# Kernel tuning notes

Hardware: AMD Instinct MI355X
Metric: run time of the kernel (lower is better)

Reference implementation:

```python
import jax, jax.numpy as jnp
import numpy as np

B, T, C = 2, 2048, 1024
H = 16
HD = C // H  # head_size = 64
FF = 2 * C   # ffwd_size default = n_embd * 2
EPS = float(jnp.finfo(jnp.float32).eps)  # torch RMSNorm eps=None -> finfo eps


def rmsnorm(x, g):
    # torch.nn.RMSNorm: x / sqrt(mean(x^2) + eps) * weight
    ms = jnp.mean(jnp.square(x), axis=-1, keepdims=True)
    return x * jax.lax.rsqrt(ms + EPS) * g


def setup_inputs() -> dict:
    key = jax.random.key(0)
    ks = jax.random.split(key, 12)
    s_in = 1.0 / np.sqrt(C)
    s_ff = 1.0 / np.sqrt(FF)
    return {
        "target": jax.random.normal(ks[0], (B, T, C), dtype=jnp.float32),
        # per-head projections, torch Linear layout [out, in] stacked over heads: [H, HD, C]
        "wq": jax.random.uniform(ks[1], (H, HD, C), jnp.float32, -s_in, s_in),
        "wk": jax.random.uniform(ks[2], (H, HD, C), jnp.float32, -s_in, s_in),
        "wv": jax.random.uniform(ks[3], (H, HD, C), jnp.float32, -s_in, s_in),
        "w_proj": jax.random.uniform(ks[4], (C, H * HD), jnp.float32, -s_in, s_in),
        "b_proj": jax.random.uniform(ks[5], (C,), jnp.float32, -s_in, s_in),
        "w1": jax.random.uniform(ks[6], (FF, C), jnp.float32, -s_in, s_in),
        "b1": jax.random.uniform(ks[7], (FF,), jnp.float32, -s_in, s_in),
        "w2": jax.random.uniform(ks[8], (C, FF), jnp.float32, -s_ff, s_ff),
        "b2": jax.random.uniform(ks[9], (C,), jnp.float32, -s_ff, s_ff),
        "g1": jnp.ones((C,), jnp.float32),
        "g2": jnp.ones((C,), jnp.float32),
    }


def reference(target, wq, wk, wv, w_proj, b_proj, w1, b1, w2, b2, g1, g2):
    x = rmsnorm(target, g1)
    # q,k,v: [B,H,T,HD]
    q = jnp.einsum("btc,hdc->bhtd", x, wq)
    k = jnp.einsum("btc,hdc->bhtd", x, wk)
    v = jnp.einsum("btc,hdc->bhtd", x, wv)
    scale = HD ** -0.5
    wei = jnp.einsum("bhtd,bhsd->bhts", q, k) * scale  # [B,H,T,T]
    causal = jnp.tril(jnp.ones((T, T), dtype=bool))
    wei = jnp.where(causal, wei, -jnp.inf)
    wei = jax.nn.softmax(wei, axis=-1)
    attn = jnp.einsum("bhts,bhsd->bhtd", wei, v)  # [B,H,T,HD]
    attn = attn.transpose(0, 2, 1, 3).reshape(B, T, H * HD)  # concat heads
    attn = attn @ w_proj.T + b_proj
    target = target + attn
    y = rmsnorm(target, g2)
    h = jax.nn.gelu(y @ w1.T + b1, approximate=False)  # torch nn.GELU default = exact
    ff = h @ w2.T + b2
    return target + ff
```

## Files before the change

kernel.cpp:

```cpp
#include <hip/hip_runtime.h>
#include <math.h>

#define B_  2
#define T_  2048
#define C_  1024
#define H_  16
#define HD_ 64
#define FF_ 2048
#define EPS_ 1.1920929e-07f

typedef __attribute__((ext_vector_type(8))) short short8;
typedef __attribute__((ext_vector_type(4))) float f32x4;

__device__ __forceinline__ unsigned short f2bf(float f) {
    unsigned u = __float_as_uint(f);
    u += 0x7fffu + ((u >> 16) & 1u);
    return (unsigned short)(u >> 16);
}
__device__ __forceinline__ float bf2f(unsigned short u) {
    return __uint_as_float(((unsigned)u) << 16);
}

__global__ void prep_kernel(const float* __restrict__ wq, const float* __restrict__ wk,
                            const float* __restrict__ wv, const float* __restrict__ wp,
                            const float* __restrict__ w1, const float* __restrict__ w2,
                            unsigned short* __restrict__ wb,
                            const float* __restrict__ x, const float* __restrict__ g,
                            unsigned short* __restrict__ y) {
    int tid = threadIdx.x;
    if (blockIdx.x < 8192) {
        size_t i = ((size_t)blockIdx.x * 256 + tid) * 4;
        const float* src; size_t off = i;
        if      (i < 1048576u)  { src = wq; }
        else if (i < 2097152u)  { src = wk; off = i - 1048576u; }
        else if (i < 3145728u)  { src = wv; off = i - 2097152u; }
        else if (i < 4194304u)  { src = wp; off = i - 3145728u; }
        else if (i < 6291456u)  { src = w1; off = i - 4194304u; }
        else                    { src = w2; off = i - 6291456u; }
        float4 v4 = *(const float4*)(src + off);
        ushort4 o4;
        o4.x = f2bf(v4.x); o4.y = f2bf(v4.y); o4.z = f2bf(v4.z); o4.w = f2bf(v4.w);
        *(ushort4*)(wb + i) = o4;
    } else {
        int row = blockIdx.x - 8192;
        const float4* xr = (const float4*)(x + (size_t)row * C_);
        float4 xv = xr[tid];
        float ss = xv.x * xv.x + xv.y * xv.y + xv.z * xv.z + xv.w * xv.w;
        #pragma unroll
        for (int m = 32; m >= 1; m >>= 1) ss += __shfl_xor(ss, m, 64);
        __shared__ float sred[4];
        if ((tid & 63) == 0) sred[tid >> 6] = ss;
        __syncthreads();
        float tot = sred[0] + sred[1] + sred[2] + sred[3];
        float r = rsqrtf(tot * (1.0f / C_) + EPS_);
        float4 gv = ((const float4*)g)[tid];
        ushort4 o;
        o.x = f2bf(xv.x * r * gv.x);
        o.y = f2bf(xv.y * r * gv.y);
        o.z = f2bf(xv.z * r * gv.z);
        o.w = f2bf(xv.w * r * gv.w);
        *((ushort4*)(y + (size_t)row * C_) + tid) = o;
    }
}

__global__ void rmsnorm_bf16_kernel(const float* __restrict__ x, const float* __restrict__ g,
                                    unsigned short* __restrict__ y) {
    int row = blockIdx.x;
    int tid = threadIdx.x;
    const float4* xr = (const float4*)(x + (size_t)row * C_);
    float4 xv = xr[tid];
    float ss = xv.x * xv.x + xv.y * xv.y + xv.z * xv.z + xv.w * xv.w;
    #pragma unroll
    for (int m = 32; m >= 1; m >>= 1) ss += __shfl_xor(ss, m, 64);
    __shared__ float sred[4];
    if ((tid & 63) == 0) sred[tid >> 6] = ss;
    __syncthreads();
    float tot = sred[0] + sred[1] + sred[2] + sred[3];
    float r = rsqrtf(tot * (1.0f / C_) + EPS_);
    float4 gv = ((const float4*)g)[tid];
    ushort4 o;
    o.x = f2bf(xv.x * r * gv.x);
    o.y = f2bf(xv.y * r * gv.y);
    o.z = f2bf(xv.z * r * gv.z);
    o.w = f2bf(xv.w * r * gv.w);
    *((ushort4*)(y + (size_t)row * C_) + tid) = o;
}

template <int TM, int ACT, bool BIAS, bool RES, bool OBF16, int ROUTE>
__global__ __launch_bounds__(256) void mfma_gemm(
        const unsigned short* __restrict__ A, const unsigned short* __restrict__ W,
        const float* __restrict__ bias, const float* __restrict__ resid,
        void* __restrict__ O0, void* __restrict__ O1, void* __restrict__ O2,
        int M, int N, int K) {
    constexpr int ACH = TM / 8;
    constexpr int NCH = (ACH + 16) / 4;
    constexpr int MI  = TM / 32;
    __shared__ short As[2 * TM * 32];
    __shared__ short Bs[2 * 128 * 32];
    const int tid  = threadIdx.x;
    const int w    = tid >> 6, lane = tid & 63;
    const int tileN = blockIdx.x * 128, tileM = blockIdx.y * TM;

    const unsigned short* gsrc[NCH];
    short* ldst[NCH];
    #pragma unroll
    for (int i2 = 0; i2 < NCH; ++i2) {
        int c = w * NCH + i2;
        if (c < ACH) {
            int kh = c / (ACH / 2), lc = c % (ACH / 2);
            gsrc[i2] = A + (size_t)(tileM + lc * 16 + (lane >> 2)) * K + kh * 32 + (lane & 3) * 8;
            ldst[i2] = As + c * 512;
        } else {
            int c2 = c - ACH;
            int kh = c2 >> 3, lc = c2 & 7;
            gsrc[i2] = W + (size_t)(tileN + lc * 16 + (lane >> 2)) * K + kh * 32 + (lane & 3) * 8;
            ldst[i2] = Bs + c2 * 512;
        }
    }

    f32x4 acc[MI][4];
    const f32x4 zed = {0.f, 0.f, 0.f, 0.f};
    #pragma unroll
    for (int i = 0; i < MI; ++i)
        #pragma unroll
        for (int j = 0; j < 4; ++j) acc[i][j] = zed;

    const int wm = (w >> 1) * (TM / 2), wn = (w & 1) * 64;
    const int frow = lane & 15, koff = (lane >> 4) * 8;

    for (int k0 = 0; k0 < K; k0 += 64) {
        #pragma unroll
        for (int i2 = 0; i2 < NCH; ++i2)
            __builtin_amdgcn_global_load_lds(
                (const __attribute__((address_space(1))) unsigned*)(gsrc[i2] + k0),
                (__attribute__((address_space(3))) unsigned*)ldst[i2], 16, 0, 0);
        __syncthreads();

        #pragma unroll
        for (int kh = 0; kh < 2; ++kh) {
            short8 af[MI], bfr[4];
            #pragma unroll
            for (int i = 0; i < MI; ++i)
                af[i] = *(const short8*)(As + kh * TM * 32 + (wm + i * 16 + frow) * 32 + koff);
            #pragma unroll
            for (int j = 0; j < 4; ++j)
                bfr[j] = *(const short8*)(Bs + kh * 128 * 32 + (wn + j * 16 + frow) * 32 + koff);
            #pragma unroll
            for (int i = 0; i < MI; ++i)
                #pragma unroll
                for (int j = 0; j < 4; ++j)
                    acc[i][j] = __builtin_amdgcn_mfma_f32_16x16x32_bf16(af[i], bfr[j], acc[i][j], 0, 0, 0);
        }
        __syncthreads();
    }

    const int ecol = lane & 15, erow = (lane >> 4) * 4;
    const int zone = ROUTE ? (tileN >> 10) : 0;
    #pragma unroll
    for (int j = 0; j < 4; ++j) {
        int n = tileN + wn + j * 16 + ecol;
        float bv = BIAS ? bias[n] : 0.f;
        int nl = ROUTE ? (n & 1023) : n;
        #pragma unroll
        for (int i = 0; i < MI; ++i) {
            int mbase = tileM + wm + i * 16 + erow;
            #pragma unroll
            for (int r = 0; r < 4; ++r) {
                float val = acc[i][j][r] + bv;
                if (ACT == 1) val = 0.5f * val * (1.0f + erff(val * 0.70710678118654752f));
                int mrow = mbase + r;
                if (ROUTE) {
                    if (zone == 0) {
                        ((unsigned short*)O0)[(size_t)mrow * 1024 + nl] = f2bf(val * 0.18033688011112042f);
                    } else if (zone == 1) {
                        ((unsigned short*)O1)[(size_t)mrow * 1024 + nl] = f2bf(val);
                    } else {
                        int bb = mrow >> 11, tt = mrow & 2047;
                        int hh = nl >> 6, dd = nl & 63;
                        ((unsigned short*)O2)[((size_t)((bb * 16 + hh) * 64 + dd)) * 2048 + tt] = f2bf(val);
                    }
                } else {
                    size_t idx = (size_t)mrow * N + n;
                    if (RES) val += resid[idx];
                    if (OBF16) ((unsigned short*)O0)[idx] = f2bf(val);
                    else       ((float*)O0)[idx] = val;
                }
            }
        }
    }
}

__global__ __launch_bounds__(256) void flash_mfma_kernel(
        const unsigned short* __restrict__ q, const unsigned short* __restrict__ k,
        const unsigned short* __restrict__ vT, unsigned short* __restrict__ out) {
    __shared__ unsigned short KsA[64 * 64];
    __shared__ unsigned short VtA[64 * 64];
    __shared__ unsigned short KsB[64 * 64];
    __shared__ unsigned short VtB[64 * 64];
    __shared__ unsigned short Ps[2 * 4 * 16 * 40];

    const int tid  = threadIdx.x;
    const int w    = tid >> 6, lane = tid & 63;
    const int quad = lane >> 4, l15 = lane & 15;
    const int bh = blockIdx.x;
    const int pair = blockIdx.y;
    const int h = bh & (H_ - 1);
    const int b = bh >> 4;

    const size_t qkbase = (size_t)b * T_ * C_ + h * HD_;
    const size_t vbase  = (size_t)(b * H_ + h) * HD_ * T_;

    short8 QB[2];
    f32x4 O[4];
    const f32x4 zed = {0.f, 0.f, 0.f, 0.f};
    float l_i = 0.f;
    int qt = 0, qg = 0;

    const int psoff = w * 640 + l15 * 40;
    const int r8 = lane >> 3, c7 = lane & 7;
    const int cswz = (c7 ^ r8) * 8;
    const int swz15 = (l15 & 7);
    const int kc = (quad ^ swz15) * 8;

    auto stageKV = [&](unsigned short* Ksb, unsigned short* Vtb, int st_) {
        const int s0_ = st_ * 64;
        #pragma unroll
        for (int c = 0; c < 2; ++c) {
            const int row = w * 16 + c * 8 + r8;
            const unsigned short* gk = k + qkbase + (size_t)(s0_ + row) * C_ + cswz;
            __builtin_amdgcn_global_load_lds(
                (const __attribute__((address_space(1))) unsigned*)gk,
                (__attribute__((address_space(3))) unsigned*)(Ksb + (w * 16 + c * 8) * 64), 16, 0, 0);
            const unsigned short* gv = vT + vbase + (size_t)row * T_ + s0_ + cswz;
            __builtin_amdgcn_global_load_lds(
                (const __attribute__((address_space(1))) unsigned*)gv,
                (__attribute__((address_space(3))) unsigned*)(Vtb + (w * 16 + c * 8) * 64), 16, 0, 0);
        }
    };

    auto computeTile = [&](const unsigned short* Ksb, const unsigned short* Vtb, int st_) {
        const bool diag = (st_ == qt);
        const int s0_ = st_ * 64;
        f32x4 Sacc[4];
        #pragma unroll
        for (int i = 0; i < 4; ++i) {
            const unsigned short* kr = Ksb + (i * 16 + l15) * 64;
            short8 KA0 = *(const short8*)(kr + kc);
            short8 KA1 = *(const short8*)(kr + (kc ^ 32));
            Sacc[i] = __builtin_amdgcn_mfma_f32_16x16x32_bf16(KA0, QB[0], zed, 0, 0, 0);
            Sacc[i] = __builtin_amdgcn_mfma_f32_16x16x32_bf16(KA1, QB[1], Sacc[i], 0, 0, 0);
        }
        float vals[16];
        #pragma unroll
        for (int i = 0; i < 4; ++i)
            #pragma unroll
            for (int r = 0; r < 4; ++r) {
                float e = __builtin_amdgcn_exp2f(Sacc[i][r]);
                if (diag) {
                    int sg = s0_ + i * 16 + quad * 4 + r;
                    e = (sg > qg) ? 0.f : e;
                }
                vals[i * 4 + r] = e;
            }
        float rs = 0.f;
        #pragma unroll
        for (int i = 0; i < 16; ++i) rs += vals[i];
        rs += __shfl_xor(rs, 16, 64);
        rs += __shfl_xor(rs, 32, 64);
        l_i += rs;

        #pragma unroll
        for (int i = 0; i < 4; ++i) {
            const int sb = i >> 1, u = i & 1;
            uint2 pw;
            pw.x = (unsigned)f2bf(vals[i * 4 + 0]) | ((unsigned)f2bf(vals[i * 4 + 1]) << 16);
            pw.y = (unsigned)f2bf(vals[i * 4 + 2]) | ((unsigned)f2bf(vals[i * 4 + 3]) << 16);
            *(uint2*)&Ps[sb * 2560 + psoff + 16 * u + quad * 4] = pw;
        }

        short8 PA0 = *(const short8*)&Ps[psoff + quad * 8];
        short8 PA1 = *(const short8*)&Ps[2560 + psoff + quad * 8];
        __builtin_amdgcn_s_setprio(1);
        #pragma unroll
        for (int dt = 0; dt < 4; ++dt) {
            const unsigned short* vr = Vtb + (16 * dt + l15) * 64;
            short8 VB0 = *(const short8*)(vr + ((quad ^ swz15) * 8));
            short8 VB1 = *(const short8*)(vr + (((4 + quad) ^ swz15) * 8));
            O[dt] = __builtin_amdgcn_mfma_f32_16x16x32_bf16(PA0, VB0, O[dt], 0, 0, 0);
            O[dt] = __builtin_amdgcn_mfma_f32_16x16x32_bf16(PA1, VB1, O[dt], 0, 0, 0);
        }
        __builtin_amdgcn_s_setprio(0);
    };

    #pragma unroll 1
    for (int half = 0; half < 2; ++half) {
        qt = half ? (T_ / 64 - 1 - pair) : pair;
        qg = qt * 64 + w * 16 + l15;
        {
            const unsigned short* qp = q + qkbase + (size_t)(qt * 64 + w * 16 + l15) * C_;
            QB[0] = *(const short8*)(qp + quad * 8);
            QB[1] = *(const short8*)(qp + 32 + quad * 8);
        }
        #pragma unroll
        for (int dt = 0; dt < 4; ++dt) O[dt] = zed;
        l_i = 0.f;

        stageKV(KsA, VtA, 0);
        __syncthreads();
        int st = 0;
        for (;;) {
            if (st + 1 <= qt) stageKV(KsB, VtB, st + 1);
            computeTile(KsA, VtA, st);
            __syncthreads();
            ++st; if (st > qt) break;
            if (st + 1 <= qt) stageKV(KsA, VtA, st + 1);
            computeTile(KsB, VtB, st);
            __syncthreads();
            ++st; if (st > qt) break;
        }

        f32x4 inv;
        #pragma unroll
        for (int r = 0; r < 4; ++r) inv[r] = 1.0f / __shfl(l_i, quad * 4 + r, 64);
        #pragma unroll
        for (int dt = 0; dt < 4; ++dt)
            #pragma unroll
            for (int r = 0; r < 4; ++r) {
                int row = qt * 64 + w * 16 + quad * 4 + r;
                int col = h * HD_ + dt * 16 + l15;
                out[((size_t)(b * T_ + row)) * C_ + col] = f2bf(O[dt][r] * inv[r]);
            }
    }
}

extern "C" void kernel_launch(void* const* d_in, const int* in_sizes, int n_in,
                              void* d_out, int out_size, void* d_ws, size_t ws_size,
                              hipStream_t stream) {
    const float* target = (const float*)d_in[0];
    const float* wq     = (const float*)d_in[1];
    const float* wk     = (const float*)d_in[2];
    const float* wv     = (const float*)d_in[3];
    const float* w_proj = (const float*)d_in[4];
    const float* b_proj = (const float*)d_in[5];
    const float* w1     = (const float*)d_in[6];
    const float* b1     = (const float*)d_in[7];
    const float* w2     = (const float*)d_in[8];
    const float* b2     = (const float*)d_in[9];
    const float* g1     = (const float*)d_in[10];
    const float* g2     = (const float*)d_in[11];
    float* out = (float*)d_out;

    char* ws = (char*)d_ws;
    const size_t MB = 1u << 20;
    unsigned short* xn = (unsigned short*)(ws);
    unsigned short* q  = (unsigned short*)(ws + 8 * MB);
    unsigned short* k  = (unsigned short*)(ws + 16 * MB);
    unsigned short* vt = (unsigned short*)(ws + 24 * MB);
    float*          x2 = (float*)(ws + 32 * MB);
    unsigned short* wb = (unsigned short*)(ws + 48 * MB);
    unsigned short* y  = q;
    unsigned short* hb = k;

    unsigned short* wqkv_b = wb;
    unsigned short* wp_b   = wb + 3145728u;
    unsigned short* w1_b   = wb + 4194304u;
    unsigned short* w2_b   = wb + 6291456u;

    const int M = B_ * T_;

    prep_kernel<<<12288, 256, 0, stream>>>(wq, wk, wv, w_proj, w1, w2, wb, target, g1, xn);

    mfma_gemm<128, 0, false, false, true, 1><<<dim3(24, M / 128), 256, 0, stream>>>(
        xn, wqkv_b, nullptr, nullptr, q, k, vt, M, 3072, C_);

    flash_mfma_kernel<<<dim3(B_ * H_, T_ / 128), 256, 0, stream>>>(q, k, vt, xn);

    mfma_gemm<64, 0, true, true, false, 0><<<dim3(C_ / 128, M / 64), 256, 0, stream>>>(
        xn, wp_b, b_proj, target, x2, nullptr, nullptr, M, C_, C_);

    rmsnorm_bf16_kernel<<<M, 256, 0, stream>>>(x2, g2, y);

    mfma_gemm<64, 1, true, false, true, 0><<<dim3(FF_ / 128, M / 64), 256, 0, stream>>>(
        y, w1_b, b1, nullptr, hb, nullptr, nullptr, M, FF_, C_);

    mfma_gemm<64, 0, true, true, false, 0><<<dim3(C_ / 128, M / 64), 256, 0, stream>>>(
        hb, w2_b, b2, x2, out, nullptr, nullptr, M, C_, FF_);
}
```

Baseline: 285.5 us.

## Split flash attention into one q-tile per block with reverse scheduling

```diff
diff --git a/kernel.cpp b/kernel.cpp
--- a/kernel.cpp
+++ b/kernel.cpp
@@ -11,6 +11,7 @@
 
 typedef __attribute__((ext_vector_type(8))) short short8;
 typedef __attribute__((ext_vector_type(4))) float f32x4;
+typedef __attribute__((ext_vector_type(2))) __bf16 bf16x2v;
 
 __device__ __forceinline__ unsigned short f2bf(float f) {
     unsigned u = __float_as_uint(f);
@@ -19,6 +20,12 @@
 }
 __device__ __forceinline__ float bf2f(unsigned short u) {
     return __uint_as_float(((unsigned)u) << 16);
+}
+__device__ __forceinline__ unsigned pk2bf(float a, float b) {
+    bf16x2v v;
+    v[0] = (__bf16)a;
+    v[1] = (__bf16)b;
+    return __builtin_bit_cast(unsigned, v);
 }
 
 __global__ void prep_kernel(const float* __restrict__ wq, const float* __restrict__ wk,
@@ -190,20 +197,20 @@
     }
 }
 
-__global__ __launch_bounds__(256) void flash_mfma_kernel(
+__global__ __launch_bounds__(256, 4) void flash_mfma_kernel(
         const unsigned short* __restrict__ q, const unsigned short* __restrict__ k,
         const unsigned short* __restrict__ vT, unsigned short* __restrict__ out) {
     __shared__ unsigned short KsA[64 * 64];
     __shared__ unsigned short VtA[64 * 64];
     __shared__ unsigned short KsB[64 * 64];
     __shared__ unsigned short VtB[64 * 64];
-    __shared__ unsigned short Ps[2 * 4 * 16 * 40];
+    __shared__ unsigned short Ps[4 * 16 * 40];
 
     const int tid  = threadIdx.x;
     const int w    = tid >> 6, lane = tid & 63;
     const int quad = lane >> 4, l15 = lane & 15;
     const int bh = blockIdx.x;
-    const int pair = blockIdx.y;
+    const int qt = (gridDim.y - 1) - blockIdx.y;
     const int h = bh & (H_ - 1);
     const int b = bh >> 4;
 
@@ -211,11 +218,19 @@
     const size_t vbase  = (size_t)(b * H_ + h) * HD_ * T_;
 
     short8 QB[2];
+    {
+        const unsigned short* qp = q + qkbase + (size_t)(qt * 64 + w * 16 + l15) * C_;
+        QB[0] = *(const short8*)(qp + quad * 8);
+        QB[1] = *(const short8*)(qp + 32 + quad * 8);
+    }
+
     f32x4 O[4];
     const f32x4 zed = {0.f, 0.f, 0.f, 0.f};
+    #pragma unroll
+    for (int dt = 0; dt < 4; ++dt) O[dt] = zed;
     float l_i = 0.f;
-    int qt = 0, qg = 0;
-
+
+    const int qg = qt * 64 + w * 16 + l15;
     const int psoff = w * 640 + l15 * 40;
     const int r8 = lane >> 3, c7 = lane & 7;
     const int cswz = (c7 ^ r8) * 8;
@@ -269,68 +284,61 @@
         rs += __shfl_xor(rs, 32, 64);
         l_i += rs;
 
-        #pragma unroll
-        for (int i = 0; i < 4; ++i) {
-            const int sb = i >> 1, u = i & 1;
-            uint2 pw;
-            pw.x = (unsigned)f2bf(vals[i * 4 + 0]) | ((unsigned)f2bf(vals[i * 4 + 1]) << 16);
-            pw.y = (unsigned)f2bf(vals[i * 4 + 2]) | ((unsigned)f2bf(vals[i * 4 + 3]) << 16);
-            *(uint2*)&Ps[sb * 2560 + psoff + 16 * u + quad * 4] = pw;
-        }
-
+        uint2 p0, p1;
+        p0.x = pk2bf(vals[0], vals[1]);  p0.y = pk2bf(vals[2], vals[3]);
+        p1.x = pk2bf(vals[4], vals[5]);  p1.y = pk2bf(vals[6], vals[7]);
+        *(uint2*)&Ps[psoff + quad * 4]      = p0;
+        *(uint2*)&Ps[psoff + 16 + quad * 4] = p1;
         short8 PA0 = *(const short8*)&Ps[psoff + quad * 8];
-        short8 PA1 = *(const short8*)&Ps[2560 + psoff + quad * 8];
+
+        uint2 p2, p3;
+        p2.x = pk2bf(vals[8], vals[9]);   p2.y = pk2bf(vals[10], vals[11]);
+        p3.x = pk2bf(vals[12], vals[13]); p3.y = pk2bf(vals[14], vals[15]);
+        *(uint2*)&Ps[psoff + quad * 4]      = p2;
+        *(uint2*)&Ps[psoff + 16 + quad * 4] = p3;
+
         __builtin_amdgcn_s_setprio(1);
         #pragma unroll
         for (int dt = 0; dt < 4; ++dt) {
             const unsigned short* vr = Vtb + (16 * dt + l15) * 64;
             short8 VB0 = *(const short8*)(vr + ((quad ^ swz15) * 8));
+            O[dt] = __builtin_amdgcn_mfma_f32_16x16x32_bf16(PA0, VB0, O[dt], 0, 0, 0);
+        }
+        short8 PA1 = *(const short8*)&Ps[psoff + quad * 8];
+        #pragma unroll
+        for (int dt = 0; dt < 4; ++dt) {
+            const unsigned short* vr = Vtb + (16 * dt + l15) * 64;
             short8 VB1 = *(const short8*)(vr + (((4 + quad) ^ swz15) * 8));
-            O[dt] = __builtin_amdgcn_mfma_f32_16x16x32_bf16(PA0, VB0, O[dt], 0, 0, 0);
             O[dt] = __builtin_amdgcn_mfma_f32_16x16x32_bf16(PA1, VB1, O[dt], 0, 0, 0);
         }
         __builtin_amdgcn_s_setprio(0);
     };
 
-    #pragma unroll 1
-    for (int half = 0; half < 2; ++half) {
-        qt = half ? (T_ / 64 - 1 - pair) : pair;
-        qg = qt * 64 + w * 16 + l15;
-        {
-            const unsigned short* qp = q + qkbase + (size_t)(qt * 64 + w * 16 + l15) * C_;
-            QB[0] = *(const short8*)(qp + quad * 8);
-            QB[1] = *(const short8*)(qp + 32 + quad * 8);
-        }
-        #pragma unroll
-        for (int dt = 0; dt < 4; ++dt) O[dt] = zed;
-        l_i = 0.f;
-
-        stageKV(KsA, VtA, 0);
-        __syncthreads();
-        int st = 0;
-        for (;;) {
-            if (st + 1 <= qt) stageKV(KsB, VtB, st + 1);
-            computeTile(KsA, VtA, st);
-            __syncthreads();
-            ++st; if (st > qt) break;
-            if (st + 1 <= qt) stageKV(KsA, VtA, st + 1);
-            computeTile(KsB, VtB, st);
-            __syncthreads();
-            ++st; if (st > qt) break;
-        }
-
-        f32x4 inv;
-        #pragma unroll
-        for (int r = 0; r < 4; ++r) inv[r] = 1.0f / __shfl(l_i, quad * 4 + r, 64);
-        #pragma unroll
-        for (int dt = 0; dt < 4; ++dt)
-            #pragma unroll
-            for (int r = 0; r < 4; ++r) {
-                int row = qt * 64 + w * 16 + quad * 4 + r;
-                int col = h * HD_ + dt * 16 + l15;
-                out[((size_t)(b * T_ + row)) * C_ + col] = f2bf(O[dt][r] * inv[r]);
-            }
-    }
+    stageKV(KsA, VtA, 0);
+    __syncthreads();
+    int st = 0;
+    for (;;) {
+        if (st + 1 <= qt) stageKV(KsB, VtB, st + 1);
+        computeTile(KsA, VtA, st);
+        __syncthreads();
+        ++st; if (st > qt) break;
+        if (st + 1 <= qt) stageKV(KsA, VtA, st + 1);
+        computeTile(KsB, VtB, st);
+        __syncthreads();
+        ++st; if (st > qt) break;
+    }
+
+    f32x4 inv;
+    #pragma unroll
+    for (int r = 0; r < 4; ++r) inv[r] = 1.0f / __shfl(l_i, quad * 4 + r, 64);
+    #pragma unroll
+    for (int dt = 0; dt < 4; ++dt)
+        #pragma unroll
+        for (int r = 0; r < 4; ++r) {
+            int row = qt * 64 + w * 16 + quad * 4 + r;
+            int col = h * HD_ + dt * 16 + l15;
+            out[((size_t)(b * T_ + row)) * C_ + col] = f2bf(O[dt][r] * inv[r]);
+        }
 }
 
 extern "C" void kernel_launch(void* const* d_in, const int* in_sizes, int n_in,
@@ -373,7 +381,7 @@
     mfma_gemm<128, 0, false, false, true, 1><<<dim3(24, M / 128), 256, 0, stream>>>(
         xn, wqkv_b, nullptr, nullptr, q, k, vt, M, 3072, C_);
 
-    flash_mfma_kernel<<<dim3(B_ * H_, T_ / 128), 256, 0, stream>>>(q, k, vt, xn);
+    flash_mfma_kernel<<<dim3(B_ * H_, T_ / 64), 256, 0, stream>>>(q, k, vt, xn);
 
     mfma_gemm<64, 0, true, true, false, 0><<<dim3(C_ / 128, M / 64), 256, 0, stream>>>(
         xn, wp_b, b_proj, target, x2, nullptr, nullptr, M, C_, C_);
```

After: 278.8 us. -2.3%, faster.
